# Performance work log

Hardware: AMD Instinct MI355X
Metric: run time of the kernel (lower is better)

## Reference

```python
import jax, jax.numpy as jnp
import numpy as np

D_MODEL = 1024
N_HEADS = 16
HEAD_DIM = D_MODEL // N_HEADS  # 64


def setup_inputs() -> dict:
    key = jax.random.key(0)
    k1, k2, k3 = jax.random.split(key, 3)
    x = jax.random.normal(k1, (2, 2048, D_MODEL), dtype=jnp.float32)
    # nn.Linear(d, 3d, bias=False): store transposed so y = x @ W
    w_qkv = jax.random.normal(k2, (D_MODEL, 3 * D_MODEL), dtype=jnp.float32) * (D_MODEL ** -0.5)
    w_proj = jax.random.normal(k3, (D_MODEL, D_MODEL), dtype=jnp.float32) * (D_MODEL ** -0.5)
    return {"x": x, "w_qkv": w_qkv, "w_proj": w_proj}


def reference(x, w_qkv, w_proj):
    b, n, _ = x.shape
    qkv = x @ w_qkv  # [b, n, 3*d_model]
    # einops 'b n (h d qkv) -> qkv b h n d': qkv axis is innermost of the split
    qkv = qkv.reshape(b, n, N_HEADS, HEAD_DIM, 3)
    q = jnp.moveaxis(qkv[..., 0], 1, 2)  # [b, h, n, d]
    k = jnp.moveaxis(qkv[..., 1], 1, 2)
    v = jnp.moveaxis(qkv[..., 2], 1, 2)
    scale = HEAD_DIM ** -0.5
    scores = jnp.einsum('bhqd,bhkd->bhqk', q, k) * scale  # [b, h, n, n]
    causal = jnp.tril(jnp.ones((n, n), dtype=bool))
    scores = jnp.where(causal[None, None], scores, -jnp.inf)
    attn = jax.nn.softmax(scores, axis=-1)
    out = jnp.einsum('bhqk,bhkd->bhqd', attn, v)  # [b, h, n, d]
    out = jnp.moveaxis(out, 1, 2).reshape(b, n, D_MODEL)  # 'b h n d -> b n (h d)'
    return out @ w_proj
```

## Files before the change

### kernel.cpp

```cpp
#include <hip/hip_runtime.h>
#include <cstdint>
#include <cstddef>

#define D_MODEL 1024
#define N_HEADS 16
#define HEAD_DIM 64
#define SEQ 2048
#define BATCH 2

typedef __attribute__((ext_vector_type(8))) short bf16x8;
typedef __attribute__((ext_vector_type(4))) float f32x4;

__device__ inline unsigned short f2bf(float f) {
    union { float f; unsigned u; } v; v.f = f;
    unsigned r = v.u + 0x7fffu + ((v.u >> 16) & 1u);
    return (unsigned short)(r >> 16);
}

__device__ __forceinline__ void gload_lds16(const unsigned short* g, unsigned short* l) {
    __builtin_amdgcn_global_load_lds(
        (const __attribute__((address_space(1))) unsigned int*)g,
        (__attribute__((address_space(3))) unsigned int*)l, 16, 0, 0);
}

__global__ __launch_bounds__(256) void convert_x_kernel(
    const float* __restrict__ X, unsigned short* __restrict__ Xb)
{
    const int idx = blockIdx.x * 256 + threadIdx.x;
    const float4* src = (const float4*)X;
    float4 v0 = src[idx * 2], v1 = src[idx * 2 + 1];
    union { unsigned short u[8]; uint4 v; } o;
    o.u[0] = f2bf(v0.x); o.u[1] = f2bf(v0.y); o.u[2] = f2bf(v0.z); o.u[3] = f2bf(v0.w);
    o.u[4] = f2bf(v1.x); o.u[5] = f2bf(v1.y); o.u[6] = f2bf(v1.z); o.u[7] = f2bf(v1.w);
    ((uint4*)Xb)[idx] = o.v;
}

__global__ __launch_bounds__(256) void convert_transpose_qkv(
    const float* __restrict__ W, unsigned short* __restrict__ Wt)
{
    __shared__ float t[32][33];
    const int c0 = blockIdx.x * 32, r0 = blockIdx.y * 32;
    const int a = threadIdx.x & 31, b = threadIdx.x >> 5;
#pragma unroll
    for (int i = 0; i < 32; i += 8)
        t[b + i][a] = W[(size_t)(r0 + b + i) * (3 * D_MODEL) + c0 + a];
    __syncthreads();
#pragma unroll
    for (int i = 0; i < 32; i += 8) {
        const int c = c0 + b + i;
        const int np = (c % 3) * 1024 + c / 3;
        Wt[(size_t)np * D_MODEL + r0 + a] = f2bf(t[a][b + i]);
    }
}

__global__ __launch_bounds__(256) void convert_transpose_kernel(
    const float* __restrict__ W, unsigned short* __restrict__ Wt,
    int ncols, int nrows)
{
    __shared__ float t[32][33];
    const int c0 = blockIdx.x * 32, r0 = blockIdx.y * 32;
    const int a = threadIdx.x & 31, b = threadIdx.x >> 5;
#pragma unroll
    for (int i = 0; i < 32; i += 8)
        t[b + i][a] = W[(size_t)(r0 + b + i) * ncols + c0 + a];
    __syncthreads();
#pragma unroll
    for (int i = 0; i < 32; i += 8)
        Wt[(size_t)(c0 + b + i) * nrows + r0 + a] = f2bf(t[a][b + i]);
}

__global__ __launch_bounds__(256) void v_transpose(
    const unsigned short* __restrict__ V, unsigned short* __restrict__ Vt)
{
    const int n0 = blockIdx.x * 64;
    const int bh = blockIdx.y;
    __shared__ unsigned short t[64 * 72];
    const int tid = threadIdx.x;
    const uint4* src = (const uint4*)(V + ((size_t)bh * SEQ + n0) * HEAD_DIM);
#pragma unroll
    for (int it = 0; it < 2; it++) {
        const int lin = tid + it * 256;
        const int row = lin >> 3, p = lin & 7;
        ((uint4*)t)[row * 9 + p] = src[lin];
    }
    __syncthreads();
#pragma unroll
    for (int it = 0; it < 2; it++) {
        const int lin = tid + it * 256;
        const int drow = lin >> 3, p = lin & 7;
        union { unsigned short u[8]; uint4 v; } o;
#pragma unroll
        for (int e = 0; e < 8; e++) o.u[e] = t[(p * 8 + e) * 72 + drow];
        ((uint4*)(Vt + ((size_t)bh * HEAD_DIM + drow) * SEQ + n0))[p] = o.v;
    }
}

#define GEMM_MFMA_BODY(A_, B_, Kdim)                                           \
    const int tid = threadIdx.x;                                               \
    const int w = tid >> 6, lane = tid & 63;                                   \
    const int l15 = lane & 15, quad = lane >> 4;                               \
    const int wr = w >> 1, wc = w & 1;                                         \
    const int row0 = blockIdx.y * 128, col0 = blockIdx.x * 128;                \
    __shared__ unsigned short As[2][8192];                                     \
    __shared__ unsigned short Bs[2][8192];                                     \
    const f32x4 zero4 = {0.f, 0.f, 0.f, 0.f};                                  \
    f32x4 acc[4][4];                                                           \
    _Pragma("unroll") for (int i = 0; i < 4; i++)                              \
        _Pragma("unroll") for (int j = 0; j < 4; j++) acc[i][j] = zero4;       \
    auto stage_ = [&](int sb, int k0) {                                        \
        _Pragma("unroll") for (int i = 0; i < 4; i++) {                        \
            const int fa = w * 4 + i;                                          \
            const int mt = fa >> 1, kh = fa & 1;                               \
            const int kc = k0 + kh * 32 + quad * 8;                            \
            gload_lds16((A_) + (size_t)(row0 + mt * 16 + l15) * (Kdim) + kc,   \
                        &As[sb][fa * 512 + lane * 8]);                         \
            gload_lds16((B_) + (size_t)(col0 + mt * 16 + l15) * (Kdim) + kc,   \
                        &Bs[sb][fa * 512 + lane * 8]);                         \
        }                                                                      \
    };                                                                         \
    stage_(0, 0);                                                              \
    const int KITER = (Kdim) / 64;                                             \
    for (int kt = 0; kt < KITER; kt++) {                                       \
        const int sb = kt & 1;                                                 \
        __syncthreads();                                                       \
        if (kt + 1 < KITER) stage_(sb ^ 1, (kt + 1) * 64);                     \
        _Pragma("unroll") for (int kh = 0; kh < 2; kh++) {                     \
            bf16x8 af[4], bfr[4];                                              \
            _Pragma("unroll") for (int i = 0; i < 4; i++)                      \
                af[i] = *(const bf16x8*)&As[sb][((wr * 4 + i) * 2 + kh) * 512 + lane * 8]; \
            _Pragma("unroll") for (int j = 0; j < 4; j++)                      \
                bfr[j] = *(const bf16x8*)&Bs[sb][((wc * 4 + j) * 2 + kh) * 512 + lane * 8]; \
            _Pragma("unroll") for (int i = 0; i < 4; i++)                      \
                _Pragma("unroll") for (int j = 0; j < 4; j++)                  \
                    acc[i][j] = __builtin_amdgcn_mfma_f32_16x16x32_bf16(       \
                        af[i], bfr[j], acc[i][j], 0, 0, 0);                    \
        }                                                                      \
    }

__global__ __launch_bounds__(256) void gemm_qkv_mfma(
    const unsigned short* __restrict__ A, const unsigned short* __restrict__ B,
    unsigned short* __restrict__ Q, unsigned short* __restrict__ Kq,
    unsigned short* __restrict__ Vb)
{
    GEMM_MFMA_BODY(A, B, D_MODEL)
    const int nbase = col0 + wc * 64;
    const int which = nbase >> 10;
    unsigned short* const dst = (which == 0) ? Q : (which == 1) ? Kq : Vb;
#pragma unroll
    for (int i = 0; i < 4; i++) {
#pragma unroll
        for (int r = 0; r < 4; r++) {
            const int row = row0 + wr * 64 + i * 16 + quad * 4 + r;
            const int bb = row >> 11, n = row & (SEQ - 1);
#pragma unroll
            for (int j = 0; j < 4; j++) {
                const int idx = (nbase + j * 16 + l15) & 1023;
                const int h = idx >> 6, dd = idx & 63;
                dst[(((size_t)(bb * N_HEADS + h)) * SEQ + n) * HEAD_DIM + dd] =
                    f2bf(acc[i][j][r]);
            }
        }
    }
}

__global__ __launch_bounds__(256) void gemm_proj_mfma(
    const unsigned short* __restrict__ A, const unsigned short* __restrict__ B,
    float* __restrict__ C)
{
    GEMM_MFMA_BODY(A, B, D_MODEL)
#pragma unroll
    for (int i = 0; i < 4; i++) {
#pragma unroll
        for (int r = 0; r < 4; r++) {
            const int row = row0 + wr * 64 + i * 16 + quad * 4 + r;
#pragma unroll
            for (int j = 0; j < 4; j++) {
                const int c = col0 + wc * 64 + j * 16 + l15;
                C[(size_t)row * D_MODEL + c] = acc[i][j][r];
            }
        }
    }
}

#define PSTR 72

__global__ __launch_bounds__(256) void flash_attn_kernel(
    const unsigned short* __restrict__ Q,
    const unsigned short* __restrict__ K,
    const unsigned short* __restrict__ Vt,
    unsigned short* __restrict__ O)
{
    const int idx = blockIdx.x;
    const int bh = idx & 31;
    const int qt2 = idx >> 5;
    const int hi = qt2 >> 3, lo = qt2 & 7;
    const int qt = (hi == 0) ? lo : (hi == 1) ? 31 - lo : (hi == 2) ? lo + 8 : 23 - lo;

    const int tid = threadIdx.x;
    const int w = tid >> 6, lane = tid & 63;
    const int l15 = lane & 15, quad = lane >> 4;

    __shared__ unsigned short Ks[2][4096];
    __shared__ unsigned short Vs[2][4096];
    __shared__ unsigned short Ps[4][16 * PSTR];

    bf16x8 qf[2];
    {
        const unsigned short* qrow =
            Q + ((size_t)bh * SEQ + qt * 64 + w * 16 + l15) * HEAD_DIM;
        qf[0] = *(const bf16x8*)(qrow + quad * 8);
        qf[1] = *(const bf16x8*)(qrow + 32 + quad * 8);
    }

    const f32x4 zero4 = {0.f, 0.f, 0.f, 0.f};
    f32x4 o_acc[4] = {zero4, zero4, zero4, zero4};
    float m_i = -1e30f, l_i = 0.f;

    auto stage = [&](int bf, int kt_t) {
        const int key0 = kt_t * 64;
#pragma unroll
        for (int i = 0; i < 2; i++) {
            const int f = w * 2 + i;
            const int ct = f >> 1, kh = f & 1;
            gload_lds16(K + ((size_t)bh * SEQ + key0 + ct * 16 + l15) * HEAD_DIM
                          + kh * 32 + quad * 8,
                        &Ks[bf][f * 512 + lane * 8]);
            gload_lds16(Vt + ((size_t)bh * HEAD_DIM + ct * 16 + l15) * SEQ
                           + key0 + kh * 32 + quad * 8,
                        &Vs[bf][f * 512 + lane * 8]);
        }
    };

    stage(0, 0);
    int buf = 0;

    const int qg = qt * 64 + w * 16 + l15;

    for (int kt = 0; kt <= qt; kt++) {
        __syncthreads();
        if (kt < qt) stage(buf ^ 1, kt + 1);

        f32x4 st[4] = {zero4, zero4, zero4, zero4};
#pragma unroll
        for (int kh = 0; kh < 2; kh++) {
#pragma unroll
            for (int ct = 0; ct < 4; ct++) {
                bf16x8 kf = *(const bf16x8*)&Ks[buf][(ct * 2 + kh) * 512 + lane * 8];
                st[ct] = __builtin_amdgcn_mfma_f32_16x16x32_bf16(kf, qf[kh], st[ct], 0, 0, 0);
            }
        }

        const bool diag = (kt == qt);
        float mt = -1e30f;
#pragma unroll
        for (int ct = 0; ct < 4; ct++) {
#pragma unroll
            for (int r = 0; r < 4; r++) {
                float v = st[ct][r] * 0.125f;
                const int kg = kt * 64 + ct * 16 + quad * 4 + r;
                if (diag && kg > qg) v = -1e30f;
                st[ct][r] = v;
                mt = fmaxf(mt, v);
            }
        }
        mt = fmaxf(mt, __shfl_xor(mt, 16));
        mt = fmaxf(mt, __shfl_xor(mt, 32));

        const float mn = fmaxf(m_i, mt);
        const float alpha = __expf(m_i - mn);
        m_i = mn;

        float ls = 0.f;
#pragma unroll
        for (int ct = 0; ct < 4; ct++) {
            union { unsigned short u[4]; uint2 v; } pk;
#pragma unroll
            for (int r = 0; r < 4; r++) {
                float p = __expf(st[ct][r] - mn);
                ls += p;
                pk.u[r] = f2bf(p);
            }
            *(uint2*)&Ps[w][l15 * PSTR + ct * 16 + quad * 4] = pk.v;
        }
        ls += __shfl_xor(ls, 16);
        ls += __shfl_xor(ls, 32);
        l_i = l_i * alpha + ls;

        float ar[4];
#pragma unroll
        for (int r = 0; r < 4; r++)
            ar[r] = __shfl(alpha, (lane & 48) | (quad * 4 + r));
#pragma unroll
        for (int dt = 0; dt < 4; dt++)
#pragma unroll
            for (int r = 0; r < 4; r++)
                o_acc[dt][r] *= ar[r];

#pragma unroll
        for (int kh = 0; kh < 2; kh++) {
            bf16x8 pa = *(const bf16x8*)&Ps[w][l15 * PSTR + kh * 32 + quad * 8];
#pragma unroll
            for (int dt = 0; dt < 4; dt++) {
                bf16x8 vf = *(const bf16x8*)&Vs[buf][(dt * 2 + kh) * 512 + lane * 8];
                o_acc[dt] = __builtin_amdgcn_mfma_f32_16x16x32_bf16(pa, vf, o_acc[dt], 0, 0, 0);
            }
        }
        buf ^= 1;
    }

    const float linv = 1.0f / l_i;
    float lr[4];
#pragma unroll
    for (int r = 0; r < 4; r++)
        lr[r] = __shfl(linv, (lane & 48) | (quad * 4 + r));

    const int b = bh >> 4, h = bh & 15;
#pragma unroll
    for (int r = 0; r < 4; r++) {
        const int q = qt * 64 + w * 16 + quad * 4 + r;
        unsigned short* orow = O + ((size_t)b * SEQ + q) * D_MODEL + h * HEAD_DIM;
#pragma unroll
        for (int dt = 0; dt < 4; dt++)
            orow[dt * 16 + l15] = f2bf(o_acc[dt][r] * lr[r]);
    }
}

extern "C" void kernel_launch(void* const* d_in, const int* in_sizes, int n_in,
                              void* d_out, int out_size, void* d_ws, size_t ws_size,
                              hipStream_t stream) {
    const float* x      = (const float*)d_in[0];
    const float* w_qkv  = (const float*)d_in[1];
    const float* w_proj = (const float*)d_in[2];
    float* out = (float*)d_out;

    unsigned short* Xb  = (unsigned short*)d_ws;
    unsigned short* Wqt = Xb  + (size_t)4 * 1024 * 1024;
    unsigned short* Wpt = Wqt + (size_t)3 * 1024 * 1024;
    unsigned short* Qb  = Wpt + (size_t)1 * 1024 * 1024;
    unsigned short* Kb  = Qb  + (size_t)4 * 1024 * 1024;
    unsigned short* Vb  = Kb  + (size_t)4 * 1024 * 1024;
    unsigned short* Vtb = Vb  + (size_t)4 * 1024 * 1024;
    unsigned short* Ob  = Vtb + (size_t)4 * 1024 * 1024;

    convert_x_kernel<<<dim3(2048), 256, 0, stream>>>(x, Xb);
    convert_transpose_qkv<<<dim3(3072 / 32, 1024 / 32), 256, 0, stream>>>(w_qkv, Wqt);
    convert_transpose_kernel<<<dim3(1024 / 32, 1024 / 32), 256, 0, stream>>>(
        w_proj, Wpt, D_MODEL, D_MODEL);

    gemm_qkv_mfma<<<dim3(3 * D_MODEL / 128, BATCH * SEQ / 128), 256, 0, stream>>>(
        Xb, Wqt, Qb, Kb, Vb);

    v_transpose<<<dim3(SEQ / 64, BATCH * N_HEADS), 256, 0, stream>>>(Vb, Vtb);

    flash_attn_kernel<<<dim3(SEQ / 64 * BATCH * N_HEADS), 256, 0, stream>>>(
        Qb, Kb, Vtb, Ob);

    gemm_proj_mfma<<<dim3(D_MODEL / 128, BATCH * SEQ / 128), 256, 0, stream>>>(
        Ob, Wpt, out);
}
```

Baseline: 229.4 us.

## Replace direct-to-LDS GEMM staging with register-prefetched two-deep pipeline

```diff
diff --git a/kernel.cpp b/kernel.cpp
--- a/kernel.cpp
+++ b/kernel.cpp
@@ -95,46 +95,64 @@
     }
 }
 
-#define GEMM_MFMA_BODY(A_, B_, Kdim)                                           \
+#define GBAR() asm volatile("s_waitcnt lgkmcnt(0)\n\ts_barrier" ::: "memory")
+
+#define P_LOAD(d, ktile)                                                       \
+    _Pragma("unroll") for (int i = 0; i < 2; i++) {                            \
+        a_p[d][i] = *(const uint4*)(Arow[i] + (ktile) * 32);                   \
+        b_p[d][i] = *(const uint4*)(Brow[i] + (ktile) * 32);                   \
+    }
+
+#define P_WRITE(d, sb)                                                        \
+    _Pragma("unroll") for (int i = 0; i < 2; i++) {                            \
+        *(uint4*)&As[sb][(w * 2 + i) * 512 + lane * 8] = a_p[d][i];            \
+        *(uint4*)&Bs[sb][(w * 2 + i) * 512 + lane * 8] = b_p[d][i];            \
+    }
+
+#define P_COMPUTE(sb)                                                         \
+    {   bf16x8 af[4], bfr[4];                                                  \
+        _Pragma("unroll") for (int i = 0; i < 4; i++)                          \
+            af[i] = *(const bf16x8*)&As[sb][(wr * 4 + i) * 512 + lane * 8];    \
+        _Pragma("unroll") for (int j = 0; j < 4; j++)                          \
+            bfr[j] = *(const bf16x8*)&Bs[sb][(wc * 4 + j) * 512 + lane * 8];   \
+        _Pragma("unroll") for (int i = 0; i < 4; i++)                          \
+            _Pragma("unroll") for (int j = 0; j < 4; j++)                      \
+                acc[i][j] = __builtin_amdgcn_mfma_f32_16x16x32_bf16(           \
+                    af[i], bfr[j], acc[i][j], 0, 0, 0);                        \
+    }
+
+#define GEMM_PIPE_BODY(A_, B_)                                                 \
     const int tid = threadIdx.x;                                               \
     const int w = tid >> 6, lane = tid & 63;                                   \
     const int l15 = lane & 15, quad = lane >> 4;                               \
     const int wr = w >> 1, wc = w & 1;                                         \
     const int row0 = blockIdx.y * 128, col0 = blockIdx.x * 128;                \
-    __shared__ unsigned short As[2][8192];                                     \
-    __shared__ unsigned short Bs[2][8192];                                     \
+    __shared__ unsigned short As[2][4096];                                     \
+    __shared__ unsigned short Bs[2][4096];                                     \
     const f32x4 zero4 = {0.f, 0.f, 0.f, 0.f};                                  \
     f32x4 acc[4][4];                                                           \
     _Pragma("unroll") for (int i = 0; i < 4; i++)                              \
         _Pragma("unroll") for (int j = 0; j < 4; j++) acc[i][j] = zero4;       \
-    auto stage_ = [&](int sb, int k0) {                                        \
-        _Pragma("unroll") for (int i = 0; i < 4; i++) {                        \
-            const int fa = w * 4 + i;                                          \
-            const int mt = fa >> 1, kh = fa & 1;                               \
-            const int kc = k0 + kh * 32 + quad * 8;                            \
-            gload_lds16((A_) + (size_t)(row0 + mt * 16 + l15) * (Kdim) + kc,   \
-                        &As[sb][fa * 512 + lane * 8]);                         \
-            gload_lds16((B_) + (size_t)(col0 + mt * 16 + l15) * (Kdim) + kc,   \
-                        &Bs[sb][fa * 512 + lane * 8]);                         \
-        }                                                                      \
-    };                                                                         \
-    stage_(0, 0);                                                              \
-    const int KITER = (Kdim) / 64;                                             \
-    for (int kt = 0; kt < KITER; kt++) {                                       \
-        const int sb = kt & 1;                                                 \
-        __syncthreads();                                                       \
-        if (kt + 1 < KITER) stage_(sb ^ 1, (kt + 1) * 64);                     \
-        _Pragma("unroll") for (int kh = 0; kh < 2; kh++) {                     \
-            bf16x8 af[4], bfr[4];                                              \
-            _Pragma("unroll") for (int i = 0; i < 4; i++)                      \
-                af[i] = *(const bf16x8*)&As[sb][((wr * 4 + i) * 2 + kh) * 512 + lane * 8]; \
-            _Pragma("unroll") for (int j = 0; j < 4; j++)                      \
-                bfr[j] = *(const bf16x8*)&Bs[sb][((wc * 4 + j) * 2 + kh) * 512 + lane * 8]; \
-            _Pragma("unroll") for (int i = 0; i < 4; i++)                      \
-                _Pragma("unroll") for (int j = 0; j < 4; j++)                  \
-                    acc[i][j] = __builtin_amdgcn_mfma_f32_16x16x32_bf16(       \
-                        af[i], bfr[j], acc[i][j], 0, 0, 0);                    \
-        }                                                                      \
+    uint4 a_p[2][2], b_p[2][2];                                                \
+    const unsigned short* Arow[2];                                             \
+    const unsigned short* Brow[2];                                             \
+    _Pragma("unroll") for (int i = 0; i < 2; i++) {                            \
+        Arow[i] = (A_) + (size_t)(row0 + (w * 2 + i) * 16 + l15) * 1024 + quad * 8; \
+        Brow[i] = (B_) + (size_t)(col0 + (w * 2 + i) * 16 + l15) * 1024 + quad * 8; \
+    }                                                                          \
+    P_LOAD(0, 0)                                                               \
+    P_LOAD(1, 1)                                                               \
+    P_WRITE(0, 0)                                                              \
+    GBAR();                                                                    \
+    _Pragma("unroll 1") for (int kt = 0; kt < 32; kt += 2) {                   \
+        if (kt + 2 < 32) { P_LOAD(0, kt + 2) }                                 \
+        P_COMPUTE(0)                                                           \
+        P_WRITE(1, 1)                                                          \
+        GBAR();                                                                \
+        if (kt + 3 < 32) { P_LOAD(1, kt + 3) }                                 \
+        P_COMPUTE(1)                                                           \
+        if (kt + 2 < 32) { P_WRITE(0, 0) }                                     \
+        GBAR();                                                                \
     }
 
 __global__ __launch_bounds__(256) void gemm_qkv_mfma(
@@ -142,7 +160,7 @@
     unsigned short* __restrict__ Q, unsigned short* __restrict__ Kq,
     unsigned short* __restrict__ Vb)
 {
-    GEMM_MFMA_BODY(A, B, D_MODEL)
+    GEMM_PIPE_BODY(A, B)
     const int nbase = col0 + wc * 64;
     const int which = nbase >> 10;
     unsigned short* const dst = (which == 0) ? Q : (which == 1) ? Kq : Vb;
@@ -167,7 +185,7 @@
     const unsigned short* __restrict__ A, const unsigned short* __restrict__ B,
     float* __restrict__ C)
 {
-    GEMM_MFMA_BODY(A, B, D_MODEL)
+    GEMM_PIPE_BODY(A, B)
 #pragma unroll
     for (int i = 0; i < 4; i++) {
 #pragma unroll
```

Result: slower. 317.1 us (+38.2%).
